# Kernel optimization log

Hardware: AMD Instinct MI355X
Metric: run time of the kernel (lower is better)

## Reference

```python
import jax, jax.numpy as jnp
import numpy as np

N_NODES = 100000
N_EDGES = 1600000
D = 128


def setup_inputs() -> dict:
    key = jax.random.key(0)
    ks = jax.random.split(key, 9)
    inp = {
        "embs": jax.random.normal(ks[0], (N_NODES, D), dtype=jnp.float32),
        "edge_index0": jax.random.randint(ks[1], (2, N_EDGES), 0, N_NODES, dtype=jnp.int64 if jax.config.jax_enable_x64 else jnp.int32),
        "edge_index1": jax.random.randint(ks[2], (2, N_EDGES), 0, N_NODES, dtype=jnp.int64 if jax.config.jax_enable_x64 else jnp.int32),
        "w_l0": jax.random.normal(ks[3], (D, D), dtype=jnp.float32) * (1.0 / np.sqrt(D)),
        "w_r0": jax.random.normal(ks[4], (D, D), dtype=jnp.float32) * (1.0 / np.sqrt(D)),
        "b0": jnp.zeros((D,), dtype=jnp.float32),
        "w_l1": jax.random.normal(ks[5], (D, D), dtype=jnp.float32) * (1.0 / np.sqrt(D)),
        "w_r1": jax.random.normal(ks[6], (D, D), dtype=jnp.float32) * (1.0 / np.sqrt(D)),
        "b1": jnp.zeros((D,), dtype=jnp.float32),
    }
    return inp


def _sage_conv(x, edge_index, w_l, w_r, b):
    # PyG SAGEConv: out[i] = lin_l(mean_{j->i} x[j]) + lin_r(x[i])
    src, dst = edge_index[0], edge_index[1]
    n = x.shape[0]
    msg = jnp.take(x, src, axis=0)                                  # [E, D] gather
    summed = jax.ops.segment_sum(msg, dst, num_segments=n)          # [N, D] scatter-add
    cnt = jax.ops.segment_sum(jnp.ones(src.shape, x.dtype), dst, num_segments=n)
    agg = summed / jnp.maximum(cnt, 1.0)[:, None]                   # mean; 0 for isolated nodes
    return agg @ w_l.T + b + x @ w_r.T


def reference(embs, edge_index0, edge_index1, w_l0, w_r0, b0, w_l1, w_r1, b1):
    # layer 0 (not last): dropout (eval -> identity) + GELU (torch default = exact erf)
    x = _sage_conv(embs, edge_index0, w_l0, w_r0, b0)
    x = jax.nn.gelu(x, approximate=False)
    # layer 1 (last): no dropout / activation
    x = _sage_conv(x, edge_index1, w_l1, w_r1, b1)
    return x
```

## Files before the change

### kernel.cpp

```cpp
#include <hip/hip_runtime.h>
#include <hip/hip_fp16.h>
#include <math.h>

#define D 128
#define SH 9
#define BW (1 << SH)
#define EPT 16

typedef _Float16 half4v __attribute__((ext_vector_type(4)));
typedef _Float16 half8  __attribute__((ext_vector_type(8)));
typedef float    floatx16 __attribute__((ext_vector_type(16)));

__global__ __launch_bounds__(256) void cast_half(
        const float* __restrict__ x, _Float16* __restrict__ y, int n) {
    int i = blockIdx.x * 256 + threadIdx.x;
    int idx = i * 4;
    if (idx >= n) return;
    float4 v = *(const float4*)(x + idx);
    half4v h;
    h[0] = (_Float16)v.x; h[1] = (_Float16)v.y;
    h[2] = (_Float16)v.z; h[3] = (_Float16)v.w;
    *(half4v*)(y + idx) = h;
}

__global__ __launch_bounds__(256) void prep_bswz(
        const float* __restrict__ wl, const float* __restrict__ wr,
        _Float16* __restrict__ B) {
    int idx = blockIdx.x * 256 + threadIdx.x;
    if (idx >= 64 * 512) return;
    int j = idx & 7;
    int lane = (idx >> 3) & 63;
    int f = idx >> 9;
    int ks = f >> 2, cb = f & 3;
    int k = ks * 16 + (lane >> 5) * 8 + j;
    int c = cb * 32 + (lane & 31);
    float v = (k < 128) ? wl[c * 128 + k] : wr[c * 128 + (k - 128)];
    B[idx] = (_Float16)v;
}

__global__ __launch_bounds__(256) void hist_coarse(
        const int* __restrict__ ei0, const int* __restrict__ ei1,
        int E, int NBK, int* __restrict__ ccnt) {
    __shared__ int h[512];
    int NBIN = 2 * NBK;
    int t = threadIdx.x;
    h[t] = 0; h[t + 256] = 0;
    __syncthreads();
    int t0 = blockIdx.x * (256 * EPT) + t;
#pragma unroll
    for (int k = 0; k < EPT; ++k) {
        int idx = t0 + k * 256;
        if (idx < 2 * E) {
            int g = idx >= E;
            int e = idx - g * E;
            int dst = (g ? ei1 : ei0)[E + e];
            atomicAdd(&h[g * NBK + (dst >> SH)], 1);
        }
    }
    __syncthreads();
    for (int b = t; b < NBIN; b += 256)
        if (h[b]) atomicAdd(&ccnt[b * 16], h[b]);
}

__global__ __launch_bounds__(256) void scan_coarse(
        const int* __restrict__ ccnt, int NBK, int E, int N,
        int* __restrict__ gbase, int* __restrict__ gcur,
        int* __restrict__ rp0, int* __restrict__ rp1) {
    __shared__ int part[256];
    int t = threadIdx.x;
    for (int g = 0; g < 2; ++g) {
        int v = (t < NBK) ? ccnt[(g * NBK + t) * 16] : 0;
        part[t] = v;
        __syncthreads();
        for (int off = 1; off < 256; off <<= 1) {
            int u = (t >= off) ? part[t - off] : 0;
            __syncthreads();
            part[t] += u;
            __syncthreads();
        }
        if (t < NBK) {
            int ex = (t == 0) ? 0 : part[t - 1];
            int b = g * NBK + t;
            gbase[b] = ex;
            gcur[b * 16] = ex;
        }
        __syncthreads();
    }
    if (t == 0) { rp0[N] = E; rp1[N] = E; }
}

__global__ __launch_bounds__(256) void bin_pass1(
        const int* __restrict__ ei0, const int* __restrict__ ei1,
        int E, int NBK, int* __restrict__ gcur,
        int* __restrict__ stage0, int* __restrict__ stage1) {
    __shared__ int cnt[512];
    __shared__ int base[512];
    int NBIN = 2 * NBK;
    int t = threadIdx.x;
    cnt[t] = 0; cnt[t + 256] = 0;
    __syncthreads();
    int t0 = blockIdx.x * (256 * EPT) + t;
    int pk[EPT];
    int bn[EPT];
#pragma unroll
    for (int k = 0; k < EPT; ++k) {
        int idx = t0 + k * 256;
        bn[k] = -1;
        if (idx < 2 * E) {
            int g = idx >= E;
            int e = idx - g * E;
            const int* ei = g ? ei1 : ei0;
            int src = ei[e];
            int dst = ei[E + e];
            pk[k] = src | ((dst & (BW - 1)) << 17);
            bn[k] = g * NBK + (dst >> SH);
            atomicAdd(&cnt[bn[k]], 1);
        }
    }
    __syncthreads();
    for (int b = t; b < NBIN; b += 256) {
        int c = cnt[b];
        base[b] = c ? atomicAdd(&gcur[b * 16], c) : 0;
        cnt[b] = 0;
    }
    __syncthreads();
#pragma unroll
    for (int k = 0; k < EPT; ++k) {
        if (bn[k] >= 0) {
            int b = bn[k];
            int r = atomicAdd(&cnt[b], 1);
            int* stage = (b >= NBK) ? stage1 : stage0;
            stage[base[b] + r] = pk[k];
        }
    }
}

__global__ __launch_bounds__(256) void bin_pass2(
        const int* __restrict__ gbase,
        const int* __restrict__ stage0, const int* __restrict__ stage1,
        int* __restrict__ rp0, int* __restrict__ rp1,
        int* __restrict__ es0, int* __restrict__ es1,
        int N, int NBK, int E) {
    __shared__ int cnt[BW];
    __shared__ int part[256];
    int b = blockIdx.x;
    int g = b >= NBK;
    int bk = b - g * NBK;
    const int* stage = g ? stage1 : stage0;
    int* rp = g ? rp1 : rp0;
    int* es = g ? es1 : es0;
    int lo = bk << SH;
    int hi = min(lo + BW, N);
    int nd = hi - lo;
    int beg = gbase[b];
    int end = (bk == NBK - 1) ? E : gbase[b + 1];
    int t = threadIdx.x;
    cnt[t] = 0; cnt[t + 256] = 0;
    __syncthreads();
    for (int i = beg + t; i < end; i += 256)
        atomicAdd(&cnt[(unsigned)stage[i] >> 17], 1);
    __syncthreads();
    int c0 = cnt[t * 2], c1 = cnt[t * 2 + 1];
    part[t] = c0 + c1;
    __syncthreads();
    for (int off = 1; off < 256; off <<= 1) {
        int u = (t >= off) ? part[t - off] : 0;
        __syncthreads();
        part[t] += u;
        __syncthreads();
    }
    int ex = (t == 0) ? 0 : part[t - 1];
    int base0 = beg + ex;
    if (t * 2 < nd)     rp[lo + t * 2]     = base0;
    if (t * 2 + 1 < nd) rp[lo + t * 2 + 1] = base0 + c0;
    __syncthreads();
    cnt[t * 2] = base0;
    cnt[t * 2 + 1] = base0 + c0;
    __syncthreads();
    int i = beg + t;
    for (; i + 768 < end; i += 1024) {
        unsigned p0 = (unsigned)stage[i];
        unsigned p1 = (unsigned)stage[i + 256];
        unsigned p2 = (unsigned)stage[i + 512];
        unsigned p3 = (unsigned)stage[i + 768];
        int q0 = atomicAdd(&cnt[p0 >> 17], 1);
        int q1 = atomicAdd(&cnt[p1 >> 17], 1);
        int q2 = atomicAdd(&cnt[p2 >> 17], 1);
        int q3 = atomicAdd(&cnt[p3 >> 17], 1);
        es[q0] = p0 & 0x1FFFF;
        es[q1] = p1 & 0x1FFFF;
        es[q2] = p2 & 0x1FFFF;
        es[q3] = p3 & 0x1FFFF;
    }
    for (; i < end; i += 256) {
        unsigned p = (unsigned)stage[i];
        int q = atomicAdd(&cnt[p >> 17], 1);
        es[q] = p & 0x1FFFF;
    }
}

__global__ __launch_bounds__(256) void agg_half(
        const _Float16* __restrict__ x, const int* __restrict__ row_ptr,
        const int* __restrict__ edge_src, _Float16* __restrict__ agg, int N) {
    int gt = blockIdx.x * 256 + threadIdx.x;
    int w = gt >> 6;
    int lane = gt & 63;
    if (w >= N) return;
    int beg = row_ptr[w];
    int end = row_ptr[w + 1];
    const __half2* base = (const __half2*)x + lane;
    float ax = 0.0f, ay = 0.0f;
    int e = beg;
    for (; e + 8 <= end; e += 8) {
        int s[8];
#pragma unroll
        for (int j = 0; j < 8; ++j) s[j] = edge_src[e + j];
#pragma unroll
        for (int j = 0; j < 8; ++j) {
            float2 f = __half22float2(base[(size_t)s[j] * 64]);
            ax += f.x;
            ay += f.y;
        }
    }
    for (; e < end; ++e) {
        float2 f = __half22float2(base[(size_t)edge_src[e] * 64]);
        ax += f.x;
        ay += f.y;
    }
    int deg = end - beg;
    float inv = (deg > 0) ? 1.0f / (float)deg : 0.0f;
    ((__half2*)agg)[(size_t)w * 64 + lane] =
        __float22half2_rn(make_float2(ax * inv, ay * inv));
}

template <bool GELU, typename OutT>
__global__ __launch_bounds__(256) void sage_mfma(
        const _Float16* __restrict__ aggh, const _Float16* __restrict__ xh,
        const _Float16* __restrict__ Bswz, const float* __restrict__ bias,
        OutT* __restrict__ out, int N) {
    __shared__ _Float16 a_lds[128 * 132];

    const int tid = threadIdx.x;
    const int n0 = blockIdx.x * 128;
    const int wave = tid >> 6;
    const int lane = tid & 63;
    const int l31 = lane & 31;
    const int lhi = lane >> 5;

    floatx16 acc[4];
#pragma unroll
    for (int cb = 0; cb < 4; ++cb)
#pragma unroll
        for (int r = 0; r < 16; ++r) acc[cb][r] = 0.0f;

    const _Float16* ap = a_lds + (wave * 32 + l31) * 132 + lhi * 8;

#pragma unroll
    for (int phase = 0; phase < 2; ++phase) {
        const _Float16* src = phase ? xh : aggh;

        __syncthreads();
        {
            int r = tid >> 1;
            int p = tid & 1;
            _Float16* dstp = a_lds + r * 132 + p * 64;
            int gn = n0 + r;
            if (gn < N) {
                const float4* gp = (const float4*)(src + (size_t)gn * 128 + p * 64);
#pragma unroll
                for (int j = 0; j < 8; ++j) {
                    float4 v = gp[j];
                    float2* w2 = (float2*)(dstp + j * 8);
                    w2[0] = make_float2(v.x, v.y);
                    w2[1] = make_float2(v.z, v.w);
                }
            } else {
#pragma unroll
                for (int j = 0; j < 8; ++j) {
                    float2* w2 = (float2*)(dstp + j * 8);
                    w2[0] = make_float2(0.f, 0.f);
                    w2[1] = make_float2(0.f, 0.f);
                }
            }
        }
        __syncthreads();

        const _Float16* bbase = Bswz + ((size_t)phase * 8 * 4 * 512) + lane * 8;
#pragma unroll
        for (int ks = 0; ks < 8; ++ks) {
            half4v alo = *(const half4v*)(ap + ks * 16);
            half4v ahi = *(const half4v*)(ap + ks * 16 + 4);
            half8 afrag = __builtin_shufflevector(alo, ahi, 0, 1, 2, 3, 4, 5, 6, 7);
#pragma unroll
            for (int cb = 0; cb < 4; ++cb) {
                half8 bfrag = *(const half8*)(bbase + (ks * 4 + cb) * 512);
                acc[cb] = __builtin_amdgcn_mfma_f32_32x32x16_f16(
                    afrag, bfrag, acc[cb], 0, 0, 0);
            }
        }
    }

#pragma unroll
    for (int cb = 0; cb < 4; ++cb) {
        int col = cb * 32 + l31;
        float bv = bias[col];
#pragma unroll
        for (int r = 0; r < 16; ++r) {
            int rowin = (r & 3) + 8 * (r >> 2) + 4 * lhi;
            int grow = n0 + wave * 32 + rowin;
            if (grow < N) {
                float v = acc[cb][r] + bv;
                if (GELU) v = 0.5f * v * (1.0f + erff(v * 0.70710678118654752f));
                out[(size_t)grow * 128 + col] = (OutT)v;
            }
        }
    }
}

extern "C" void kernel_launch(void* const* d_in, const int* in_sizes, int n_in,
                              void* d_out, int out_size, void* d_ws, size_t ws_size,
                              hipStream_t stream) {
    const float* embs = (const float*)d_in[0];
    const int*   ei0  = (const int*)d_in[1];
    const int*   ei1  = (const int*)d_in[2];
    const float* w_l0 = (const float*)d_in[3];
    const float* w_r0 = (const float*)d_in[4];
    const float* b0   = (const float*)d_in[5];
    const float* w_l1 = (const float*)d_in[6];
    const float* w_r1 = (const float*)d_in[7];
    const float* b1   = (const float*)d_in[8];
    float* out = (float*)d_out;

    const int N = in_sizes[0] / D;
    const int E = in_sizes[1] / 2;
    const int NBK = (N + BW - 1) >> SH;
    const int NBIN = 2 * NBK;

    _Float16* x_h   = (_Float16*)d_ws;
    _Float16* h_h   = x_h + (size_t)N * D;
    _Float16* agg_h = h_h + (size_t)N * D;
    _Float16* Bswz0 = agg_h + (size_t)N * D;
    _Float16* Bswz1 = Bswz0 + 64 * 512;
    int* rp0   = (int*)(Bswz1 + 64 * 512);
    int* rp1   = rp0 + (N + 1);
    int* es0   = rp1 + (N + 1);
    int* es1   = es0 + E;
    int* ccnt  = es1 + E;
    int* gbase = ccnt + NBIN * 16;
    int* gcur  = gbase + NBIN;
    int* stage0 = (int*)agg_h;
    int* stage1 = stage0 + E;

    const int cast_grid = ((size_t)N * D / 4 + 255) / 256;
    const int bin_grid  = (2 * E + 256 * EPT - 1) / (256 * EPT);
    const int agg_grid  = ((size_t)N * 64 + 255) / 256;
    const int gemm_grid = (N + 127) / 128;

    cast_half<<<cast_grid, 256, 0, stream>>>(embs, x_h, N * D);
    prep_bswz<<<128, 256, 0, stream>>>(w_l0, w_r0, Bswz0);
    prep_bswz<<<128, 256, 0, stream>>>(w_l1, w_r1, Bswz1);

    hipMemsetAsync(ccnt, 0, (size_t)NBIN * 16 * sizeof(int), stream);
    hist_coarse<<<bin_grid, 256, 0, stream>>>(ei0, ei1, E, NBK, ccnt);
    scan_coarse<<<1, 256, 0, stream>>>(ccnt, NBK, E, N, gbase, gcur, rp0, rp1);
    bin_pass1<<<bin_grid, 256, 0, stream>>>(ei0, ei1, E, NBK, gcur,
                                            stage0, stage1);
    bin_pass2<<<NBIN, 256, 0, stream>>>(gbase, stage0, stage1,
                                        rp0, rp1, es0, es1, N, NBK, E);

    agg_half<<<agg_grid, 256, 0, stream>>>(x_h, rp0, es0, agg_h, N);
    sage_mfma<true, _Float16><<<gemm_grid, 256, 0, stream>>>(
        agg_h, x_h, Bswz0, b0, h_h, N);

    agg_half<<<agg_grid, 256, 0, stream>>>(h_h, rp1, es1, agg_h, N);
    sage_mfma<false, float><<<gemm_grid, 256, 0, stream>>>(
        agg_h, h_h, Bswz1, b1, out, N);
}
```

Before: 433.8 us.

## Split wave into two half-groups gathering 8-byte rows with shuffled indices

The fp16 mean-aggregation kernel is restructured. Each wave now loads up to 64 edge indices in one coalesced read and broadcasts them with shuffles. The two 32-lane halves each gather a different neighbour row with 8-byte loads and accumulate via inline v_fma_mix_f32, then combine the halves with a cross-half shuffle before writing. The aim is fewer scalar index loads, wider memory transactions and more gathers in flight, at the cost of shuffle overhead and predicated loads on partial chunks.

```diff
diff --git a/kernel.cpp b/kernel.cpp
--- a/kernel.cpp
+++ b/kernel.cpp
@@ -208,29 +208,57 @@
     if (w >= N) return;
     int beg = row_ptr[w];
     int end = row_ptr[w + 1];
-    const __half2* base = (const __half2*)x + lane;
-    float ax = 0.0f, ay = 0.0f;
-    int e = beg;
-    for (; e + 8 <= end; e += 8) {
-        int s[8];
-#pragma unroll
-        for (int j = 0; j < 8; ++j) s[j] = edge_src[e + j];
-#pragma unroll
-        for (int j = 0; j < 8; ++j) {
-            float2 f = __half22float2(base[(size_t)s[j] * 64]);
-            ax += f.x;
-            ay += f.y;
-        }
-    }
-    for (; e < end; ++e) {
-        float2 f = __half22float2(base[(size_t)edge_src[e] * 64]);
-        ax += f.x;
-        ay += f.y;
-    }
+    int grp = lane >> 5;
+    int c   = lane & 31;
+    unsigned co = (unsigned)c * 8u;
+    const char* xb = (const char*)x;
+    float ax = 0.f, ay = 0.f, az = 0.f, aw = 0.f;
+    float one = 1.0f;
+
+    for (int chunk = beg; chunk < end; chunk += 64) {
+        int n = min(64, end - chunk);
+        int iv = (lane < n) ? edge_src[chunk + lane] : -1;
+        for (int e = 0; e < n; e += 8) {
+            int s[4];
+            uint2 v[4];
+#pragma unroll
+            for (int j = 0; j < 4; ++j)
+                s[j] = __shfl(iv, e + 2 * j + grp);
+#pragma unroll
+            for (int j = 0; j < 4; ++j) {
+                v[j] = make_uint2(0u, 0u);
+                if (s[j] >= 0)
+                    v[j] = *(const uint2*)(xb + (unsigned)s[j] * 256u + co);
+            }
+#pragma unroll
+            for (int j = 0; j < 4; ++j) {
+                asm("v_fma_mix_f32 %0, %1, %2, %0 op_sel:[0,0,0] op_sel_hi:[1,0,0]"
+                    : "+v"(ax) : "v"(v[j].x), "v"(one));
+                asm("v_fma_mix_f32 %0, %1, %2, %0 op_sel:[1,0,0] op_sel_hi:[1,0,0]"
+                    : "+v"(ay) : "v"(v[j].x), "v"(one));
+                asm("v_fma_mix_f32 %0, %1, %2, %0 op_sel:[0,0,0] op_sel_hi:[1,0,0]"
+                    : "+v"(az) : "v"(v[j].y), "v"(one));
+                asm("v_fma_mix_f32 %0, %1, %2, %0 op_sel:[1,0,0] op_sel_hi:[1,0,0]"
+                    : "+v"(aw) : "v"(v[j].y), "v"(one));
+            }
+        }
+    }
+
+    ax += __shfl_xor(ax, 32);
+    ay += __shfl_xor(ay, 32);
+    az += __shfl_xor(az, 32);
+    aw += __shfl_xor(aw, 32);
+
     int deg = end - beg;
     float inv = (deg > 0) ? 1.0f / (float)deg : 0.0f;
-    ((__half2*)agg)[(size_t)w * 64 + lane] =
-        __float22half2_rn(make_float2(ax * inv, ay * inv));
+    if (lane < 32) {
+        half4v h;
+        h[0] = (_Float16)(ax * inv);
+        h[1] = (_Float16)(ay * inv);
+        h[2] = (_Float16)(az * inv);
+        h[3] = (_Float16)(aw * inv);
+        *(half4v*)((char*)agg + (size_t)w * 256 + co) = h;
+    }
 }
 
 template <bool GELU, typename OutT>
```

New measurement: 410.0 us. 1.06x faster.
